# Performance work log

Measured on AMD Instinct MI355X. Metric: run time of the kernel, lower is better.

The kernel has to match this reference:

```python
import jax, jax.numpy as jnp
import numpy as np

H = 32  # num_heads
ROPE_BASE = 10000.0


def _rope(x, offset):
    # x: [B, H, S, D]; rotate-half RoPE with position offset
    B, h, S, D = x.shape
    pos = offset + jnp.arange(S, dtype=jnp.float32)              # [S]
    inv_freq = 1.0 / (ROPE_BASE ** (jnp.arange(0, D, 2, dtype=jnp.float32) / D))  # [D/2]
    ang = pos[:, None] * inv_freq[None, :]                        # [S, D/2]
    cos = jnp.concatenate([jnp.cos(ang), jnp.cos(ang)], axis=-1)  # [S, D]
    sin = jnp.concatenate([jnp.sin(ang), jnp.sin(ang)], axis=-1)  # [S, D]
    x1, x2 = x[..., : D // 2], x[..., D // 2 :]
    rot = jnp.concatenate([-x2, x1], axis=-1)
    return x * cos + rot * sin


def setup_inputs() -> dict:
    key = jax.random.key(0)
    ks = jax.random.split(key, 8)
    B, S, HD = 8, 16, 4096
    Dh = HD // H
    PAST = 4080
    inp = {
        "x": jax.random.normal(ks[0], (B, S, HD), dtype=jnp.float32),
        "past_key": jax.random.normal(ks[1], (B, H, PAST, Dh), dtype=jnp.float32),
        "past_value": jax.random.normal(ks[2], (B, H, PAST, Dh), dtype=jnp.float32),
        "Wq": jax.random.normal(ks[3], (HD, HD), dtype=jnp.float32) * 0.02,
        "bq": jnp.zeros((HD,), dtype=jnp.float32),
        "Wk": jax.random.normal(ks[4], (HD, HD), dtype=jnp.float32) * 0.02,
        "bk": jnp.zeros((HD,), dtype=jnp.float32),
        "Wv": jax.random.normal(ks[5], (HD, HD), dtype=jnp.float32) * 0.02,
        "bv": jnp.zeros((HD,), dtype=jnp.float32),
        "Wo": jax.random.normal(ks[6], (HD, HD), dtype=jnp.float32) * 0.02,
        "bo": jnp.zeros((HD,), dtype=jnp.float32),
    }
    return inp


def reference(x, past_key, past_value, Wq, bq, Wk, bk, Wv, bv, Wo, bo):
    B, S, HD = x.shape
    Dh = HD // H
    scale = Dh ** -0.5
    past_len = past_key.shape[2]

    def split_heads(t):  # [B,S,HD] -> [B,H,S,Dh]
        return t.reshape(B, S, H, Dh).transpose(0, 2, 1, 3)

    Q = split_heads(x @ Wq.T + bq)
    K = split_heads(x @ Wk.T + bk)
    V = split_heads(x @ Wv.T + bv)

    Q = _rope(Q, past_len)
    K = _rope(K, past_len)

    K = jnp.concatenate([past_key, K], axis=2)   # [B,H,past+S,Dh]
    V = jnp.concatenate([past_value, V], axis=2)

    scores = jnp.einsum("bhqd,bhkd->bhqk", Q, K) * scale
    attn = jax.nn.softmax(scores, axis=-1)       # dropout: identity in eval
    out = jnp.einsum("bhqk,bhkd->bhqd", attn, V)
    out = out.transpose(0, 2, 1, 3).reshape(B, S, HD)
    out = out @ Wo.T + bo
    return out, attn, (K, V)
```

## Files before the change

kernel.cpp:

```cpp
#include <hip/hip_runtime.h>
#include <hip/hip_bf16.h>

#define BB 8
#define SS 16
#define HH 32
#define DH 128
#define HD 4096
#define PAST 4080
#define TOT 4096
#define MM 128

#define OUT_O  0
#define ATTN_O 524288
#define K_O    17301504
#define V_O    151519232

#define QR_O 0
#define OH_O 524288
#define STATS_O 524288
#define ROWS_O  786432
#define RT_O 1048576
#define PW_O 1050624

typedef __attribute__((ext_vector_type(8))) short short8;
typedef __attribute__((ext_vector_type(4))) float f32x4;
typedef __attribute__((ext_vector_type(4))) float f4v;

static __device__ inline unsigned short f2bf(float x) {
  __hip_bfloat16 h = __float2bfloat16(x);
  return *reinterpret_cast<unsigned short*>(&h);
}

__global__ void rope_table_kernel(float* __restrict__ rt) {
  int t = threadIdx.x;
  int s = t >> 6, j = t & 63;
  double inv = exp(-((double)(2 * j) / 128.0) * log(10000.0));
  double ang = (double)(PAST + s) * inv;
  rt[t] = (float)cos(ang);
  rt[1024 + t] = (float)sin(ang);
}

#define LDP 72
__global__ __launch_bounds__(256) void gemm_mfma(
    const float* __restrict__ A, const float* __restrict__ W0,
    const float* __restrict__ W1, const float* __restrict__ W2,
    float* __restrict__ P) {
  int bx = blockIdx.x;
  int mat = bx >> 8;
  int rem = bx & 255;
  int nc = rem >> 3, ks = rem & 7;
  const float* Wm = (mat == 0) ? W0 : ((mat == 1) ? W1 : W2);
  int n0 = nc * 128;
  int tid = threadIdx.x;
  int lane = tid & 63, wid = tid >> 6;
  int wm = wid >> 1, wn = wid & 1;
  int l15 = lane & 15, l4 = lane >> 4;

  __shared__ unsigned short As[128 * LDP];
  __shared__ unsigned short Bs[128 * LDP];

  f32x4 acc[4][4];
#pragma unroll
  for (int i = 0; i < 4; ++i)
#pragma unroll
    for (int j = 0; j < 4; ++j) acc[i][j] = (f32x4){0.f, 0.f, 0.f, 0.f};

  int srow = tid >> 1;
  int skh = (tid & 1) * 32;

  for (int kt = 0; kt < 8; ++kt) {
    int k0 = ks * 512 + kt * 64;
    const float* Ap = &A[(size_t)srow * 4096 + k0 + skh];
    const float* Wp = &Wm[(size_t)(n0 + srow) * 4096 + k0 + skh];
    float4 va[8], vb[8];
#pragma unroll
    for (int i = 0; i < 8; ++i) {
      va[i] = *(const float4*)(Ap + 4 * i);
      vb[i] = *(const float4*)(Wp + 4 * i);
    }
    __syncthreads();
    unsigned short* Asp = &As[srow * LDP + skh];
    unsigned short* Bsp = &Bs[srow * LDP + skh];
#pragma unroll
    for (int i = 0; i < 8; ++i) {
      ushort4 ua, ub;
      ua.x = f2bf(va[i].x); ua.y = f2bf(va[i].y);
      ua.z = f2bf(va[i].z); ua.w = f2bf(va[i].w);
      ub.x = f2bf(vb[i].x); ub.y = f2bf(vb[i].y);
      ub.z = f2bf(vb[i].z); ub.w = f2bf(vb[i].w);
      *(ushort4*)(Asp + 4 * i) = ua;
      *(ushort4*)(Bsp + 4 * i) = ub;
    }
    __syncthreads();
#pragma unroll
    for (int s = 0; s < 2; ++s) {
      short8 af[4], bf[4];
#pragma unroll
      for (int f = 0; f < 4; ++f) {
        int ar = wm * 64 + f * 16 + l15;
        af[f] = *(const short8*)&As[ar * LDP + s * 32 + l4 * 8];
        int br = wn * 64 + f * 16 + l15;
        bf[f] = *(const short8*)&Bs[br * LDP + s * 32 + l4 * 8];
      }
#pragma unroll
      for (int i = 0; i < 4; ++i)
#pragma unroll
        for (int j = 0; j < 4; ++j)
          acc[i][j] = __builtin_amdgcn_mfma_f32_16x16x32_bf16(
              af[i], bf[j], acc[i][j], 0, 0, 0);
    }
  }

  float* Pb = P + (size_t)(mat * 8 + ks) * 524288 + n0;
#pragma unroll
  for (int i = 0; i < 4; ++i) {
#pragma unroll
    for (int j = 0; j < 4; ++j) {
      int mbase = wm * 64 + i * 16 + l4 * 4;
      int nn = wn * 64 + j * 16 + l15;
#pragma unroll
      for (int r = 0; r < 4; ++r)
        Pb[(size_t)(mbase + r) * 4096 + nn] = acc[i][j][r];
    }
  }
}

__global__ __launch_bounds__(256) void qkv_reduce(
    const float* __restrict__ P, const float* __restrict__ bq,
    const float* __restrict__ bk, const float* __restrict__ bv,
    const float* __restrict__ rt, float* __restrict__ qr,
    float* __restrict__ kout, float* __restrict__ vout) {
  int t = blockIdx.x * 256 + threadIdx.x;
  int d2 = t & 63;
  int h = (t >> 6) & 31;
  int m = (t >> 11) & 127;
  int mat = t >> 18;
  int n1 = h * 128 + d2, n2 = n1 + 64;
  const float* bias = (mat == 0) ? bq : ((mat == 1) ? bk : bv);
  float v1 = bias[n1], v2 = bias[n2];
  const float* Pm = P + (size_t)(mat * 8) * 524288 + (size_t)m * 4096;
#pragma unroll
  for (int s = 0; s < 8; ++s) {
    v1 += Pm[(size_t)s * 524288 + n1];
    v2 += Pm[(size_t)s * 524288 + n2];
  }
  int st = m & 15, b = m >> 4;
  int bh = b * 32 + h;
  if (mat == 2) {
    size_t dst = (size_t)(bh * TOT + PAST + st) * 128;
    vout[dst + d2] = v1; vout[dst + 64 + d2] = v2;
  } else {
    float c = rt[st * 64 + d2], sn = rt[1024 + st * 64 + d2];
    float o1 = v1 * c - v2 * sn;
    float o2 = v2 * c + v1 * sn;
    if (mat == 0) {
      size_t dst = (size_t)(bh * 16 + st) * 128;
      qr[dst + d2] = o1; qr[dst + 64 + d2] = o2;
    } else {
      size_t dst = (size_t)(bh * TOT + PAST + st) * 128;
      kout[dst + d2] = o1; kout[dst + 64 + d2] = o2;
    }
  }
}

__global__ __launch_bounds__(256) void scores_kernel(
    const float* __restrict__ pastk, const float* __restrict__ qr,
    float* __restrict__ kout, float* __restrict__ attn,
    float* __restrict__ stats) {
  int bh = blockIdx.x >> 5, kc = blockIdx.x & 31;
  int r0 = kc * 128;
  int tid = threadIdx.x;
  __shared__ float KsT[64][129];
  __shared__ float Qs[2048];
#pragma unroll
  for (int i = 0; i < 8; ++i)
    Qs[tid + i * 256] = qr[(size_t)bh * 2048 + tid + i * 256];

  const f4v* pk4 = (const f4v*)pastk;
  f4v* ko4 = (f4v*)kout;
  int qg = tid >> 6, lane = tid & 63;
  float acc[4][2] = {{0.f, 0.f}, {0.f, 0.f}, {0.f, 0.f}, {0.f, 0.f}};

  for (int p = 0; p < 2; ++p) {
    if (p) __syncthreads();
#pragma unroll
    for (int i = 0; i < 8; ++i) {
      int f = tid + i * 256;
      int r = f >> 4, g16 = f & 15;
      int g = g16 + p * 16;
      int row = r0 + r;
      size_t kidx = (size_t)(bh * TOT + row) * 32 + g;
      const f4v* src = (row < PAST)
          ? (pk4 + ((size_t)(bh * PAST + row) * 32 + g))
          : (const f4v*)(ko4 + kidx);
      f4v v = __builtin_nontemporal_load(src);
      if (row < PAST) __builtin_nontemporal_store(v, ko4 + kidx);
      int dl = g16 * 4;
      KsT[dl][r] = v.x; KsT[dl + 1][r] = v.y;
      KsT[dl + 2][r] = v.z; KsT[dl + 3][r] = v.w;
    }
    __syncthreads();
    int dbase = p * 64;
#pragma unroll 4
    for (int d = 0; d < 64; ++d) {
      float k0v = KsT[d][lane], k1v = KsT[d][lane + 64];
#pragma unroll
      for (int j = 0; j < 4; ++j) {
        float qv = Qs[(qg * 4 + j) * 128 + dbase + d];
        acc[j][0] = fmaf(qv, k0v, acc[j][0]);
        acc[j][1] = fmaf(qv, k1v, acc[j][1]);
      }
    }
  }
  const float scale = 0.088388347648318447f;
#pragma unroll
  for (int j = 0; j < 4; ++j) { acc[j][0] *= scale; acc[j][1] *= scale; }
#pragma unroll
  for (int j = 0; j < 4; ++j) {
    int q = qg * 4 + j;
    size_t base = (size_t)(bh * 16 + q) * 4096 + r0;
    attn[base + lane] = acc[j][0];
    attn[base + 64 + lane] = acc[j][1];
  }
#pragma unroll
  for (int j = 0; j < 4; ++j) {
    float m = fmaxf(acc[j][0], acc[j][1]);
#pragma unroll
    for (int off = 32; off; off >>= 1) m = fmaxf(m, __shfl_xor(m, off));
    float e = __expf(acc[j][0] - m) + __expf(acc[j][1] - m);
#pragma unroll
    for (int off = 32; off; off >>= 1) e += __shfl_xor(e, off);
    if (lane == 0) {
      int q = qg * 4 + j;
      size_t si = ((size_t)(bh * 16 + q) * 32 + kc) * 2;
      stats[si] = m; stats[si + 1] = e;
    }
  }
}

__global__ __launch_bounds__(256) void stats_reduce(
    const float* __restrict__ stats, float* __restrict__ rows) {
  int r = blockIdx.x * 256 + threadIdx.x;
  float m = -1e30f;
#pragma unroll
  for (int c = 0; c < 32; ++c) m = fmaxf(m, stats[((size_t)r * 32 + c) * 2]);
  float s = 0.f;
#pragma unroll
  for (int c = 0; c < 32; ++c)
    s += stats[((size_t)r * 32 + c) * 2 + 1] *
         __expf(stats[((size_t)r * 32 + c) * 2] - m);
  rows[r * 2] = m;
  rows[r * 2 + 1] = 1.f / s;
}

__global__ __launch_bounds__(256) void pv_kernel(
    const float* __restrict__ pastv, float* __restrict__ attn,
    const float* __restrict__ rows, float* __restrict__ vout,
    float* __restrict__ pvp) {
  int blk = blockIdx.x;
  int bh = blk >> 2, nc = blk & 3;
  int tid = threadIdx.x;
  int dq = tid & 31, rg = tid >> 5;
  __shared__ float atn[16][256];
  __shared__ float red[4][16][128];
  __shared__ float sm[16], si[16];
  if (tid < 16) {
    sm[tid] = rows[(bh * 16 + tid) * 2];
    si[tid] = rows[(bh * 16 + tid) * 2 + 1];
  }
  float acc[16][4];
#pragma unroll
  for (int q = 0; q < 16; ++q)
#pragma unroll
    for (int j = 0; j < 4; ++j) acc[q][j] = 0.f;

  const f4v* pv4 = (const f4v*)pastv;
  f4v* vo4 = (f4v*)vout;
  int base0 = nc * 1024;
  __syncthreads();

  for (int slab = 0; slab < 4; ++slab) {
    int kbase = base0 + slab * 256;
#pragma unroll
    for (int q = 0; q < 16; ++q) {
      size_t ai = (size_t)(bh * 16 + q) * 4096 + kbase + tid;
      float x = attn[ai];
      float p = __expf(x - sm[q]) * si[q];
      atn[q][tid] = p;
      __builtin_nontemporal_store(p, &attn[ai]);
    }
    __syncthreads();
#pragma unroll 2
    for (int it = 0; it < 32; it += 2) {
      int kk0 = it * 8 + rg, kk1 = kk0 + 8;
      int row0 = kbase + kk0, row1 = kbase + kk1;
      size_t o0 = (size_t)(bh * TOT + row0) * 32 + dq;
      size_t o1 = (size_t)(bh * TOT + row1) * 32 + dq;
      const f4v* s0 = (row0 < PAST)
          ? (pv4 + ((size_t)(bh * PAST + row0) * 32 + dq)) : (const f4v*)(vo4 + o0);
      const f4v* s1 = (row1 < PAST)
          ? (pv4 + ((size_t)(bh * PAST + row1) * 32 + dq)) : (const f4v*)(vo4 + o1);
      f4v v0 = __builtin_nontemporal_load(s0);
      f4v v1 = __builtin_nontemporal_load(s1);
      if (row0 < PAST) __builtin_nontemporal_store(v0, vo4 + o0);
      if (row1 < PAST) __builtin_nontemporal_store(v1, vo4 + o1);
#pragma unroll
      for (int q = 0; q < 16; ++q) {
        float a = atn[q][kk0];
        acc[q][0] = fmaf(a, v0.x, acc[q][0]);
        acc[q][1] = fmaf(a, v0.y, acc[q][1]);
        acc[q][2] = fmaf(a, v0.z, acc[q][2]);
        acc[q][3] = fmaf(a, v0.w, acc[q][3]);
      }
#pragma unroll
      for (int q = 0; q < 16; ++q) {
        float a = atn[q][kk1];
        acc[q][0] = fmaf(a, v1.x, acc[q][0]);
        acc[q][1] = fmaf(a, v1.y, acc[q][1]);
        acc[q][2] = fmaf(a, v1.z, acc[q][2]);
        acc[q][3] = fmaf(a, v1.w, acc[q][3]);
      }
    }
    __syncthreads();
  }
#pragma unroll
  for (int q = 0; q < 16; ++q)
#pragma unroll
    for (int j = 0; j < 4; ++j) acc[q][j] += __shfl_xor(acc[q][j], 32);
  int wid = tid >> 6;
  if ((tid & 63) < 32) {
#pragma unroll
    for (int q = 0; q < 16; ++q) {
      f4v o; o.x = acc[q][0]; o.y = acc[q][1]; o.z = acc[q][2]; o.w = acc[q][3];
      *(f4v*)&red[wid][q][dq * 4] = o;
    }
  }
  __syncthreads();
#pragma unroll
  for (int rep = 0; rep < 8; ++rep) {
    int o = tid + rep * 256;
    int q = o >> 7, dd = o & 127;
    float s = red[0][q][dd] + red[1][q][dd] + red[2][q][dd] + red[3][q][dd];
    pvp[((size_t)(bh * 4 + nc) * 16 + q) * 128 + dd] = s;
  }
}

__global__ __launch_bounds__(256) void pv_reduce(
    const float* __restrict__ pvp, float* __restrict__ oh) {
  int t = blockIdx.x * 256 + threadIdx.x;
  int dd = t & 127;
  int q = (t >> 7) & 15;
  int bh = t >> 11;
  int b = bh >> 5, h = bh & 31;
  float s = 0.f;
#pragma unroll
  for (int nc = 0; nc < 4; ++nc)
    s += pvp[((size_t)(bh * 4 + nc) * 16 + q) * 128 + dd];
  oh[(size_t)(b * 16 + q) * 4096 + h * 128 + dd] = s;
}

__global__ __launch_bounds__(256) void out_reduce(
    const float* __restrict__ P, const float* __restrict__ bo,
    float* __restrict__ out) {
  int t = blockIdx.x * 256 + threadIdx.x;
  float v = bo[t & 4095];
#pragma unroll
  for (int s = 0; s < 8; ++s) v += P[(size_t)s * 524288 + t];
  out[t] = v;
}

extern "C" void kernel_launch(void* const* d_in, const int* in_sizes, int n_in,
                              void* d_out, int out_size, void* d_ws, size_t ws_size,
                              hipStream_t stream) {
  const float* x     = (const float*)d_in[0];
  const float* pastk = (const float*)d_in[1];
  const float* pastv = (const float*)d_in[2];
  const float* Wq = (const float*)d_in[3];
  const float* bq = (const float*)d_in[4];
  const float* Wk = (const float*)d_in[5];
  const float* bk = (const float*)d_in[6];
  const float* Wv = (const float*)d_in[7];
  const float* bv = (const float*)d_in[8];
  const float* Wo = (const float*)d_in[9];
  const float* bo = (const float*)d_in[10];

  float* out  = (float*)d_out;
  float* attn = out + ATTN_O;
  float* kout = out + K_O;
  float* vout = out + V_O;

  float* ws = (float*)d_ws;
  float* qr    = ws + QR_O;
  float* oh    = ws + OH_O;
  float* stats = ws + STATS_O;
  float* rows  = ws + ROWS_O;
  float* rt    = ws + RT_O;
  float* pw    = ws + PW_O;

  rope_table_kernel<<<1, 1024, 0, stream>>>(rt);
  gemm_mfma<<<768, 256, 0, stream>>>(x, Wq, Wk, Wv, attn);
  qkv_reduce<<<3072, 256, 0, stream>>>(attn, bq, bk, bv, rt, qr, kout, vout);
  scores_kernel<<<8192, 256, 0, stream>>>(pastk, qr, kout, attn, stats);
  stats_reduce<<<16, 256, 0, stream>>>(stats, rows);
  pv_kernel<<<1024, 256, 0, stream>>>(pastv, attn, rows, vout, pw);
  pv_reduce<<<2048, 256, 0, stream>>>(pw, oh);
  gemm_mfma<<<256, 256, 0, stream>>>(oh, Wo, Wo, Wo, pw);
  out_reduce<<<2048, 256, 0, stream>>>(pw, bo, out);
}
```

Before: 643.3 us.

## Use bf16 MFMA for scores, fold stats reduce and rope table, split PV finer

```diff
diff --git a/kernel.cpp b/kernel.cpp
--- a/kernel.cpp
+++ b/kernel.cpp
@@ -18,7 +18,6 @@
 #define QR_O 0
 #define OH_O 524288
 #define STATS_O 524288
-#define ROWS_O  786432
 #define RT_O 1048576
 #define PW_O 1050624
 
@@ -30,21 +29,33 @@
   __hip_bfloat16 h = __float2bfloat16(x);
   return *reinterpret_cast<unsigned short*>(&h);
 }
-
-__global__ void rope_table_kernel(float* __restrict__ rt) {
-  int t = threadIdx.x;
-  int s = t >> 6, j = t & 63;
-  double inv = exp(-((double)(2 * j) / 128.0) * log(10000.0));
-  double ang = (double)(PAST + s) * inv;
-  rt[t] = (float)cos(ang);
-  rt[1024 + t] = (float)sin(ang);
+static __device__ inline short8 cvt8(float4 a, float4 b) {
+  short8 v;
+  v[0] = (short)f2bf(a.x); v[1] = (short)f2bf(a.y);
+  v[2] = (short)f2bf(a.z); v[3] = (short)f2bf(a.w);
+  v[4] = (short)f2bf(b.x); v[5] = (short)f2bf(b.y);
+  v[6] = (short)f2bf(b.z); v[7] = (short)f2bf(b.w);
+  return v;
 }
 
 #define LDP 72
 __global__ __launch_bounds__(256) void gemm_mfma(
     const float* __restrict__ A, const float* __restrict__ W0,
     const float* __restrict__ W1, const float* __restrict__ W2,
-    float* __restrict__ P) {
+    float* __restrict__ P, float* __restrict__ rt) {
+  if (rt != nullptr && blockIdx.x == 768) {
+    int t = threadIdx.x;
+#pragma unroll
+    for (int i = 0; i < 4; ++i) {
+      int idx = t + i * 256;
+      int s = idx >> 6, j = idx & 63;
+      double inv = exp(-((double)(2 * j) / 128.0) * log(10000.0));
+      double ang = (double)(PAST + s) * inv;
+      rt[idx] = (float)cos(ang);
+      rt[1024 + idx] = (float)sin(ang);
+    }
+    return;
+  }
   int bx = blockIdx.x;
   int mat = bx >> 8;
   int rem = bx & 255;
@@ -56,8 +67,8 @@
   int wm = wid >> 1, wn = wid & 1;
   int l15 = lane & 15, l4 = lane >> 4;
 
-  __shared__ unsigned short As[128 * LDP];
-  __shared__ unsigned short Bs[128 * LDP];
+  __shared__ __align__(16) unsigned short As[128 * LDP];
+  __shared__ __align__(16) unsigned short Bs[128 * LDP];
 
   f32x4 acc[4][4];
 #pragma unroll
@@ -82,14 +93,9 @@
     unsigned short* Asp = &As[srow * LDP + skh];
     unsigned short* Bsp = &Bs[srow * LDP + skh];
 #pragma unroll
-    for (int i = 0; i < 8; ++i) {
-      ushort4 ua, ub;
-      ua.x = f2bf(va[i].x); ua.y = f2bf(va[i].y);
-      ua.z = f2bf(va[i].z); ua.w = f2bf(va[i].w);
-      ub.x = f2bf(vb[i].x); ub.y = f2bf(vb[i].y);
-      ub.z = f2bf(vb[i].z); ub.w = f2bf(vb[i].w);
-      *(ushort4*)(Asp + 4 * i) = ua;
-      *(ushort4*)(Bsp + 4 * i) = ub;
+    for (int i = 0; i < 4; ++i) {
+      *(short8*)(Asp + 8 * i) = cvt8(va[2 * i], va[2 * i + 1]);
+      *(short8*)(Bsp + 8 * i) = cvt8(vb[2 * i], vb[2 * i + 1]);
     }
     __syncthreads();
 #pragma unroll
@@ -163,110 +169,138 @@
   }
 }
 
-__global__ __launch_bounds__(256) void scores_kernel(
+#define KST 136
+__global__ __launch_bounds__(256) void scores_mfma(
     const float* __restrict__ pastk, const float* __restrict__ qr,
     float* __restrict__ kout, float* __restrict__ attn,
     float* __restrict__ stats) {
   int bh = blockIdx.x >> 5, kc = blockIdx.x & 31;
   int r0 = kc * 128;
-  int tid = threadIdx.x;
-  __shared__ float KsT[64][129];
-  __shared__ float Qs[2048];
-#pragma unroll
-  for (int i = 0; i < 8; ++i)
-    Qs[tid + i * 256] = qr[(size_t)bh * 2048 + tid + i * 256];
+  int tid = threadIdx.x, lane = tid & 63, w = tid >> 6;
+  int l15 = lane & 15, l4 = lane >> 4;
+
+  __shared__ __align__(16) unsigned short Ks[128 * KST];
+  __shared__ __align__(16) unsigned short Qs[16 * KST];
+  __shared__ float sred[2][4][16];
 
   const f4v* pk4 = (const f4v*)pastk;
   f4v* ko4 = (f4v*)kout;
-  int qg = tid >> 6, lane = tid & 63;
-  float acc[4][2] = {{0.f, 0.f}, {0.f, 0.f}, {0.f, 0.f}, {0.f, 0.f}};
-
-  for (int p = 0; p < 2; ++p) {
-    if (p) __syncthreads();
-#pragma unroll
-    for (int i = 0; i < 8; ++i) {
-      int f = tid + i * 256;
-      int r = f >> 4, g16 = f & 15;
-      int g = g16 + p * 16;
-      int row = r0 + r;
-      size_t kidx = (size_t)(bh * TOT + row) * 32 + g;
-      const f4v* src = (row < PAST)
-          ? (pk4 + ((size_t)(bh * PAST + row) * 32 + g))
-          : (const f4v*)(ko4 + kidx);
-      f4v v = __builtin_nontemporal_load(src);
-      if (row < PAST) __builtin_nontemporal_store(v, ko4 + kidx);
-      int dl = g16 * 4;
-      KsT[dl][r] = v.x; KsT[dl + 1][r] = v.y;
-      KsT[dl + 2][r] = v.z; KsT[dl + 3][r] = v.w;
-    }
-    __syncthreads();
-    int dbase = p * 64;
-#pragma unroll 4
-    for (int d = 0; d < 64; ++d) {
-      float k0v = KsT[d][lane], k1v = KsT[d][lane + 64];
-#pragma unroll
-      for (int j = 0; j < 4; ++j) {
-        float qv = Qs[(qg * 4 + j) * 128 + dbase + d];
-        acc[j][0] = fmaf(qv, k0v, acc[j][0]);
-        acc[j][1] = fmaf(qv, k1v, acc[j][1]);
-      }
-    }
+
+#pragma unroll
+  for (int i = 0; i < 4; ++i) {
+    int p = tid + i * 256;
+    int row = p >> 3, cp = p & 7;
+    int grow = r0 + row;
+    int d4 = cp * 4;
+    size_t kidx = (size_t)(bh * TOT + grow) * 32 + d4;
+    float4 v0, v1, v2, v3;
+    if (grow < PAST) {
+      size_t sidx = (size_t)(bh * PAST + grow) * 32 + d4;
+      v0 = ((const float4*)pk4)[sidx];     v1 = ((const float4*)pk4)[sidx + 1];
+      v2 = ((const float4*)pk4)[sidx + 2]; v3 = ((const float4*)pk4)[sidx + 3];
+      __builtin_nontemporal_store(*(const f4v*)&v0, ko4 + kidx);
+      __builtin_nontemporal_store(*(const f4v*)&v1, ko4 + kidx + 1);
+      __builtin_nontemporal_store(*(const f4v*)&v2, ko4 + kidx + 2);
+      __builtin_nontemporal_store(*(const f4v*)&v3, ko4 + kidx + 3);
+    } else {
+      v0 = ((const float4*)ko4)[kidx];     v1 = ((const float4*)ko4)[kidx + 1];
+      v2 = ((const float4*)ko4)[kidx + 2]; v3 = ((const float4*)ko4)[kidx + 3];
+    }
+    unsigned short* dst = &Ks[row * KST + cp * 16];
+    *(short8*)(dst)     = cvt8(v0, v1);
+    *(short8*)(dst + 8) = cvt8(v2, v3);
+  }
+  if (tid < 128) {
+    int q = tid >> 3, cp = tid & 7;
+    const float* src = &qr[(size_t)bh * 2048 + q * 128 + cp * 16];
+    float4 a0 = *(const float4*)(src);
+    float4 a1 = *(const float4*)(src + 4);
+    float4 a2 = *(const float4*)(src + 8);
+    float4 a3 = *(const float4*)(src + 12);
+    unsigned short* dst = &Qs[q * KST + cp * 16];
+    *(short8*)(dst)     = cvt8(a0, a1);
+    *(short8*)(dst + 8) = cvt8(a2, a3);
+  }
+  __syncthreads();
+
+  f32x4 acc0 = (f32x4){0.f, 0.f, 0.f, 0.f};
+  f32x4 acc1 = (f32x4){0.f, 0.f, 0.f, 0.f};
+#pragma unroll
+  for (int s = 0; s < 4; ++s) {
+    short8 aq = *(const short8*)&Qs[l15 * KST + s * 32 + l4 * 8];
+    short8 b0 = *(const short8*)&Ks[(w * 32 + l15) * KST + s * 32 + l4 * 8];
+    short8 b1 = *(const short8*)&Ks[(w * 32 + 16 + l15) * KST + s * 32 + l4 * 8];
+    acc0 = __builtin_amdgcn_mfma_f32_16x16x32_bf16(aq, b0, acc0, 0, 0, 0);
+    acc1 = __builtin_amdgcn_mfma_f32_16x16x32_bf16(aq, b1, acc1, 0, 0, 0);
   }
   const float scale = 0.088388347648318447f;
-#pragma unroll
-  for (int j = 0; j < 4; ++j) { acc[j][0] *= scale; acc[j][1] *= scale; }
-#pragma unroll
-  for (int j = 0; j < 4; ++j) {
-    int q = qg * 4 + j;
-    size_t base = (size_t)(bh * 16 + q) * 4096 + r0;
-    attn[base + lane] = acc[j][0];
-    attn[base + 64 + lane] = acc[j][1];
-  }
-#pragma unroll
-  for (int j = 0; j < 4; ++j) {
-    float m = fmaxf(acc[j][0], acc[j][1]);
-#pragma unroll
-    for (int off = 32; off; off >>= 1) m = fmaxf(m, __shfl_xor(m, off));
-    float e = __expf(acc[j][0] - m) + __expf(acc[j][1] - m);
-#pragma unroll
-    for (int off = 32; off; off >>= 1) e += __shfl_xor(e, off);
-    if (lane == 0) {
-      int q = qg * 4 + j;
-      size_t si = ((size_t)(bh * 16 + q) * 32 + kc) * 2;
-      stats[si] = m; stats[si + 1] = e;
-    }
-  }
-}
-
-__global__ __launch_bounds__(256) void stats_reduce(
-    const float* __restrict__ stats, float* __restrict__ rows) {
-  int r = blockIdx.x * 256 + threadIdx.x;
-  float m = -1e30f;
-#pragma unroll
-  for (int c = 0; c < 32; ++c) m = fmaxf(m, stats[((size_t)r * 32 + c) * 2]);
-  float s = 0.f;
-#pragma unroll
-  for (int c = 0; c < 32; ++c)
-    s += stats[((size_t)r * 32 + c) * 2 + 1] *
-         __expf(stats[((size_t)r * 32 + c) * 2] - m);
-  rows[r * 2] = m;
-  rows[r * 2 + 1] = 1.f / s;
+  float v0[4], v1[4], mx[4], ex[4];
+#pragma unroll
+  for (int r = 0; r < 4; ++r) {
+    v0[r] = acc0[r] * scale;
+    v1[r] = acc1[r] * scale;
+    int q = l4 * 4 + r;
+    size_t base = (size_t)(bh * 16 + q) * 4096 + r0 + w * 32 + l15;
+    attn[base] = v0[r];
+    attn[base + 16] = v1[r];
+    mx[r] = fmaxf(v0[r], v1[r]);
+  }
+#pragma unroll
+  for (int r = 0; r < 4; ++r) {
+#pragma unroll
+    for (int off = 1; off < 16; off <<= 1)
+      mx[r] = fmaxf(mx[r], __shfl_xor(mx[r], off));
+    ex[r] = __expf(v0[r] - mx[r]) + __expf(v1[r] - mx[r]);
+#pragma unroll
+    for (int off = 1; off < 16; off <<= 1)
+      ex[r] += __shfl_xor(ex[r], off);
+  }
+  if (l15 == 0) {
+#pragma unroll
+    for (int r = 0; r < 4; ++r) {
+      sred[0][w][l4 * 4 + r] = mx[r];
+      sred[1][w][l4 * 4 + r] = ex[r];
+    }
+  }
+  __syncthreads();
+  if (tid < 16) {
+    float M = sred[0][0][tid];
+#pragma unroll
+    for (int ww = 1; ww < 4; ++ww) M = fmaxf(M, sred[0][ww][tid]);
+    float E = 0.f;
+#pragma unroll
+    for (int ww = 0; ww < 4; ++ww)
+      E += sred[1][ww][tid] * __expf(sred[0][ww][tid] - M);
+    size_t si = ((size_t)(bh * 16 + tid) * 32 + kc) * 2;
+    stats[si] = M; stats[si + 1] = E;
+  }
 }
 
 __global__ __launch_bounds__(256) void pv_kernel(
     const float* __restrict__ pastv, float* __restrict__ attn,
-    const float* __restrict__ rows, float* __restrict__ vout,
+    const float* __restrict__ stats, float* __restrict__ vout,
     float* __restrict__ pvp) {
   int blk = blockIdx.x;
-  int bh = blk >> 2, nc = blk & 3;
+  int bh = blk >> 3, nc = blk & 7;
   int tid = threadIdx.x;
   int dq = tid & 31, rg = tid >> 5;
-  __shared__ float atn[16][256];
-  __shared__ float red[4][16][128];
+  __shared__ __align__(16) float red[4][16][128];
+  float* atn = &red[0][0][0];
   __shared__ float sm[16], si[16];
-  if (tid < 16) {
-    sm[tid] = rows[(bh * 16 + tid) * 2];
-    si[tid] = rows[(bh * 16 + tid) * 2 + 1];
+
+  {
+    int row = tid >> 4, c0 = (tid & 15) * 2;
+    float4 s4 = *(const float4*)&stats[((size_t)(bh * 16 + row) * 32 + c0) * 2];
+    float m = fmaxf(s4.x, s4.z);
+    float e = s4.y * __expf(s4.x - m) + s4.w * __expf(s4.z - m);
+#pragma unroll
+    for (int off = 1; off < 16; off <<= 1) {
+      float mo = __shfl_xor(m, off), eo = __shfl_xor(e, off);
+      float M = fmaxf(m, mo);
+      e = e * __expf(m - M) + eo * __expf(mo - M);
+      m = M;
+    }
+    if ((tid & 15) == 0) { sm[row] = m; si[row] = 1.f / e; }
   }
   float acc[16][4];
 #pragma unroll
@@ -276,22 +310,23 @@
 
   const f4v* pv4 = (const f4v*)pastv;
   f4v* vo4 = (f4v*)vout;
-  int base0 = nc * 1024;
+  int base0 = nc * 512;
   __syncthreads();
 
   for (int slab = 0; slab < 4; ++slab) {
-    int kbase = base0 + slab * 256;
-#pragma unroll
-    for (int q = 0; q < 16; ++q) {
-      size_t ai = (size_t)(bh * 16 + q) * 4096 + kbase + tid;
-      float x = attn[ai];
-      float p = __expf(x - sm[q]) * si[q];
-      atn[q][tid] = p;
+    int kbase = base0 + slab * 128;
+#pragma unroll
+    for (int i = 0; i < 8; ++i) {
+      int idx = tid + i * 256;
+      int q = idx >> 7, k = idx & 127;
+      size_t ai = (size_t)(bh * 16 + q) * 4096 + kbase + k;
+      float p = __expf(attn[ai] - sm[q]) * si[q];
+      atn[q * 128 + k] = p;
       __builtin_nontemporal_store(p, &attn[ai]);
     }
     __syncthreads();
 #pragma unroll 2
-    for (int it = 0; it < 32; it += 2) {
+    for (int it = 0; it < 16; it += 2) {
       int kk0 = it * 8 + rg, kk1 = kk0 + 8;
       int row0 = kbase + kk0, row1 = kbase + kk1;
       size_t o0 = (size_t)(bh * TOT + row0) * 32 + dq;
@@ -300,25 +335,25 @@
           ? (pv4 + ((size_t)(bh * PAST + row0) * 32 + dq)) : (const f4v*)(vo4 + o0);
       const f4v* s1 = (row1 < PAST)
           ? (pv4 + ((size_t)(bh * PAST + row1) * 32 + dq)) : (const f4v*)(vo4 + o1);
-      f4v v0 = __builtin_nontemporal_load(s0);
-      f4v v1 = __builtin_nontemporal_load(s1);
-      if (row0 < PAST) __builtin_nontemporal_store(v0, vo4 + o0);
-      if (row1 < PAST) __builtin_nontemporal_store(v1, vo4 + o1);
+      f4v x0 = __builtin_nontemporal_load(s0);
+      f4v x1 = __builtin_nontemporal_load(s1);
+      if (row0 < PAST) __builtin_nontemporal_store(x0, vo4 + o0);
+      if (row1 < PAST) __builtin_nontemporal_store(x1, vo4 + o1);
 #pragma unroll
       for (int q = 0; q < 16; ++q) {
-        float a = atn[q][kk0];
-        acc[q][0] = fmaf(a, v0.x, acc[q][0]);
-        acc[q][1] = fmaf(a, v0.y, acc[q][1]);
-        acc[q][2] = fmaf(a, v0.z, acc[q][2]);
-        acc[q][3] = fmaf(a, v0.w, acc[q][3]);
+        float a = atn[q * 128 + kk0];
+        acc[q][0] = fmaf(a, x0.x, acc[q][0]);
+        acc[q][1] = fmaf(a, x0.y, acc[q][1]);
+        acc[q][2] = fmaf(a, x0.z, acc[q][2]);
+        acc[q][3] = fmaf(a, x0.w, acc[q][3]);
       }
 #pragma unroll
       for (int q = 0; q < 16; ++q) {
-        float a = atn[q][kk1];
-        acc[q][0] = fmaf(a, v1.x, acc[q][0]);
-        acc[q][1] = fmaf(a, v1.y, acc[q][1]);
-        acc[q][2] = fmaf(a, v1.z, acc[q][2]);
-        acc[q][3] = fmaf(a, v1.w, acc[q][3]);
+        float a = atn[q * 128 + kk1];
+        acc[q][0] = fmaf(a, x1.x, acc[q][0]);
+        acc[q][1] = fmaf(a, x1.y, acc[q][1]);
+        acc[q][2] = fmaf(a, x1.z, acc[q][2]);
+        acc[q][3] = fmaf(a, x1.w, acc[q][3]);
       }
     }
     __syncthreads();
@@ -341,7 +376,7 @@
     int o = tid + rep * 256;
     int q = o >> 7, dd = o & 127;
     float s = red[0][q][dd] + red[1][q][dd] + red[2][q][dd] + red[3][q][dd];
-    pvp[((size_t)(bh * 4 + nc) * 16 + q) * 128 + dd] = s;
+    pvp[((size_t)(bh * 8 + nc) * 16 + q) * 128 + dd] = s;
   }
 }
 
@@ -354,8 +389,8 @@
   int b = bh >> 5, h = bh & 31;
   float s = 0.f;
 #pragma unroll
-  for (int nc = 0; nc < 4; ++nc)
-    s += pvp[((size_t)(bh * 4 + nc) * 16 + q) * 128 + dd];
+  for (int nc = 0; nc < 8; ++nc)
+    s += pvp[((size_t)(bh * 8 + nc) * 16 + q) * 128 + dd];
   oh[(size_t)(b * 16 + q) * 4096 + h * 128 + dd] = s;
 }
 
@@ -393,17 +428,14 @@
   float* qr    = ws + QR_O;
   float* oh    = ws + OH_O;
   float* stats = ws + STATS_O;
-  float* rows  = ws + ROWS_O;
   float* rt    = ws + RT_O;
   float* pw    = ws + PW_O;
 
-  rope_table_kernel<<<1, 1024, 0, stream>>>(rt);
-  gemm_mfma<<<768, 256, 0, stream>>>(x, Wq, Wk, Wv, attn);
+  gemm_mfma<<<769, 256, 0, stream>>>(x, Wq, Wk, Wv, attn, rt);
   qkv_reduce<<<3072, 256, 0, stream>>>(attn, bq, bk, bv, rt, qr, kout, vout);
-  scores_kernel<<<8192, 256, 0, stream>>>(pastk, qr, kout, attn, stats);
-  stats_reduce<<<16, 256, 0, stream>>>(stats, rows);
-  pv_kernel<<<1024, 256, 0, stream>>>(pastv, attn, rows, vout, pw);
+  scores_mfma<<<8192, 256, 0, stream>>>(pastk, qr, kout, attn, stats);
+  pv_kernel<<<2048, 256, 0, stream>>>(pastv, attn, stats, vout, pw);
   pv_reduce<<<2048, 256, 0, stream>>>(pw, oh);
-  gemm_mfma<<<256, 256, 0, stream>>>(oh, Wo, Wo, Wo, pw);
+  gemm_mfma<<<256, 256, 0, stream>>>(oh, Wo, Wo, Wo, pw, nullptr);
   out_reduce<<<2048, 256, 0, stream>>>(pw, bo, out);
 }
```

After: 1.313 ms. 104% more time.
